# Kernel optimization log

Hardware: AMD Instinct MI355X
Metric: run time of the kernel (lower is better)

Reference implementation:

```python
import jax, jax.numpy as jnp
import numpy as np

COMMITMENT_COST = 0.25
NUM_EMBEDDINGS = 1024
EMBEDDING_DIM = 512  # win_size(8) * num_pellets(64)


def setup_inputs() -> dict:
    key = jax.random.key(0)
    k1, k2 = jax.random.split(key)
    inputs = jax.random.normal(k1, (64, 256, EMBEDDING_DIM), dtype=jnp.float32)
    # matches torch init: uniform_(-1/K, 1/K)
    lim = 1.0 / NUM_EMBEDDINGS
    emb_weight = jax.random.uniform(k2, (NUM_EMBEDDINGS, EMBEDDING_DIM),
                                    dtype=jnp.float32, minval=-lim, maxval=lim)
    return {"inputs": inputs, "emb_weight": emb_weight}


def reference(inputs, emb_weight):
    batch_size = inputs.shape[0]
    input_shape = inputs.shape
    flat = inputs.reshape(-1, EMBEDDING_DIM)  # [N, D]

    distances = (jnp.sum(flat * flat, axis=1, keepdims=True)
                 + jnp.sum(emb_weight * emb_weight, axis=1)
                 - 2.0 * flat @ emb_weight.T)
    encoding_indices = jnp.argmin(distances, axis=1)  # [N]

    # gather instead of one-hot matmul (same math)
    quantized = emb_weight[encoding_indices].reshape(input_shape)

    e_latent_loss = jnp.mean((jax.lax.stop_gradient(quantized) - inputs) ** 2)
    q_latent_loss = jnp.mean((quantized - jax.lax.stop_gradient(inputs)) ** 2)
    loss_vq = q_latent_loss + COMMITMENT_COST * e_latent_loss

    # straight-through estimator
    quantized = inputs + jax.lax.stop_gradient(quantized - inputs)

    encoding_indices = encoding_indices.reshape(batch_size, -1)
    return loss_vq, quantized, encoding_indices
```

## Files before the change

### kernel.cpp

```cpp
#include <hip/hip_runtime.h>
#include <cfloat>

#define NROWS  16384
#define DIM    512
#define KC     1024
#define QELEMS (NROWS * DIM)

#define NSPLIT 8
#define CHUNKS 130

typedef float  floatx4 __attribute__((ext_vector_type(4)));
typedef _Float16 half8 __attribute__((ext_vector_type(8)));
typedef _Float16 half4 __attribute__((ext_vector_type(4)));

__global__ __launch_bounds__(256) void prep_kernel(const float* __restrict__ A,
                                                   const float* __restrict__ E,
                                                   float* __restrict__ xsq,
                                                   float* __restrict__ esq,
                                                   _Float16* __restrict__ ah,
                                                   _Float16* __restrict__ al,
                                                   _Float16* __restrict__ eh,
                                                   _Float16* __restrict__ el,
                                                   unsigned long long* __restrict__ packed,
                                                   float* __restrict__ out) {
    if (blockIdx.x == 0 && threadIdx.x == 0) out[0] = 0.f;
    const int wave = threadIdx.x >> 6, lane = threadIdx.x & 63;
    const bool isA = blockIdx.x < (NROWS / 4);
    const int row = (isA ? blockIdx.x : blockIdx.x - NROWS / 4) * 4 + wave;
    const float* M = isA ? A : E;
    const float scale = isA ? 2048.0f : 65536.0f;

    const float4* Mr = (const float4*)(M + (size_t)row * DIM);
    float4 va = Mr[lane];
    float4 vb = Mr[lane + 64];
    float s = 0.f;
    s += va.x*va.x + va.y*va.y + va.z*va.z + va.w*va.w;
    s += vb.x*vb.x + vb.y*vb.y + vb.z*vb.z + vb.w*vb.w;
    #pragma unroll
    for (int off = 32; off; off >>= 1) s += __shfl_down(s, off, 64);
    if (lane == 0) {
        if (isA) { xsq[row] = s; packed[row] = ~0ULL; }
        else     { esq[row] = s; }
    }

    float xa[4] = {va.x, va.y, va.z, va.w}, xb[4] = {vb.x, vb.y, vb.z, vb.w};
    half4 ha, la, hb, lb;
    #pragma unroll
    for (int e = 0; e < 4; ++e) {
        float t = xa[e] * scale;
        _Float16 h = (_Float16)t;
        ha[e] = h; la[e] = (_Float16)(t - (float)h);
        t = xb[e] * scale;
        h = (_Float16)t;
        hb[e] = h; lb[e] = (_Float16)(t - (float)h);
    }
    _Float16* hr = (isA ? ah : eh) + (size_t)row * DIM;
    _Float16* lr = (isA ? al : el) + (size_t)row * DIM;
    ((half4*)hr)[lane]      = ha;
    ((half4*)lr)[lane]      = la;
    ((half4*)hr)[lane + 64] = hb;
    ((half4*)lr)[lane + 64] = lb;
}

__global__ __launch_bounds__(256, 3) void mfma_argmin_kernel(const _Float16* __restrict__ ah,
                                                             const _Float16* __restrict__ al,
                                                             const _Float16* __restrict__ eh,
                                                             const _Float16* __restrict__ el,
                                                             const float* __restrict__ esq,
                                                             const float* __restrict__ xsq,
                                                             unsigned long long* __restrict__ packed) {
    __shared__ half8 AhT[2][4 * CHUNKS], AlT[2][4 * CHUNKS];
    __shared__ float redv[128][2];
    __shared__ int   redi[128][2];

    const int tid = threadIdx.x;
    const int lane = tid & 63, wave = tid >> 6;
    const int wm = wave >> 1, wn = wave & 1;
    const int tx = lane & 15, qd = lane >> 4;
    const int bm = blockIdx.x & 127, bn = blockIdx.x >> 7;
    const int m0 = bm * 128, c0 = bn * 128;

    const int srow = tid >> 2, skq = tid & 3;
    const _Float16* gA  = ah + (size_t)(m0 + srow) * DIM + skq * 8;
    const _Float16* gAl = al + (size_t)(m0 + srow) * DIM + skq * 8;
    const int cw0 = skq * CHUNKS + srow, cw1 = cw0 + 64;

    const _Float16* gBh = eh + (size_t)(c0 + wn * 64 + tx) * DIM + qd * 8;
    const _Float16* gBl = el + (size_t)(c0 + wn * 64 + tx) * DIM + qd * 8;

    floatx4 acc[4][4];
    #pragma unroll
    for (int i = 0; i < 4; ++i)
        #pragma unroll
        for (int j = 0; j < 4; ++j) acc[i][j] = (floatx4){0.f, 0.f, 0.f, 0.f};

    half8 rA0 = *(const half8*)(gA);
    half8 rA1 = *(const half8*)(gA  + 64 * DIM);
    half8 rL0 = *(const half8*)(gAl);
    half8 rL1 = *(const half8*)(gAl + 64 * DIM);
    AhT[0][cw0] = rA0; AhT[0][cw1] = rA1;
    AlT[0][cw0] = rL0; AlT[0][cw1] = rL1;

    #pragma unroll 1
    for (int kt = 0; kt < DIM / 32; ++kt) {
        const int cur = kt & 1, nxt = cur ^ 1;
        const int kb = (kt + 1) * 32;
        const int ke = kt * 32;

        half8 fbh[4], fbl[4];
        #pragma unroll
        for (int j = 0; j < 4; ++j)
            fbh[j] = *(const half8*)(gBh + (size_t)j * 16 * DIM + ke);
        if (kt < DIM / 32 - 1) {
            rA0 = *(const half8*)(gA  + kb);
            rA1 = *(const half8*)(gA  + 64 * DIM + kb);
            rL0 = *(const half8*)(gAl + kb);
            rL1 = *(const half8*)(gAl + 64 * DIM + kb);
        }
        #pragma unroll
        for (int j = 0; j < 4; ++j)
            fbl[j] = *(const half8*)(gBl + (size_t)j * 16 * DIM + ke);
        __syncthreads();

        half8 fa[4];
        #pragma unroll
        for (int i = 0; i < 4; ++i)
            fa[i] = AhT[cur][qd * CHUNKS + wm * 64 + i * 16 + tx];
        #pragma unroll
        for (int i = 0; i < 4; ++i)
            #pragma unroll
            for (int j = 0; j < 4; ++j)
                acc[i][j] = __builtin_amdgcn_mfma_f32_16x16x32_f16(fa[i], fbh[j], acc[i][j], 0, 0, 0);
        #pragma unroll
        for (int i = 0; i < 4; ++i)
            #pragma unroll
            for (int j = 0; j < 4; ++j)
                acc[i][j] = __builtin_amdgcn_mfma_f32_16x16x32_f16(fa[i], fbl[j], acc[i][j], 0, 0, 0);
        #pragma unroll
        for (int i = 0; i < 4; ++i)
            fa[i] = AlT[cur][qd * CHUNKS + wm * 64 + i * 16 + tx];
        #pragma unroll
        for (int i = 0; i < 4; ++i)
            #pragma unroll
            for (int j = 0; j < 4; ++j)
                acc[i][j] = __builtin_amdgcn_mfma_f32_16x16x32_f16(fa[i], fbh[j], acc[i][j], 0, 0, 0);

        if (kt < DIM / 32 - 1) {
            AhT[nxt][cw0] = rA0; AhT[nxt][cw1] = rA1;
            AlT[nxt][cw0] = rL0; AlT[nxt][cw1] = rL1;
        }
    }

    float sqe_v[4];
    #pragma unroll
    for (int j = 0; j < 4; ++j) sqe_v[j] = esq[c0 + wn * 64 + j * 16 + tx];
    #pragma unroll
    for (int i = 0; i < 4; ++i) {
        #pragma unroll
        for (int r = 0; r < 4; ++r) {
            int rl = wm * 64 + i * 16 + qd * 4 + r;
            float sx = xsq[m0 + rl];
            float bvv = FLT_MAX; int bii = 0x7fffffff;
            #pragma unroll
            for (int j = 0; j < 4; ++j) {
                float S = sx + sqe_v[j];
                float s = S - acc[i][j][r] * (1.0f / 67108864.0f);
                int c = c0 + wn * 64 + j * 16 + tx;
                if (s < bvv || (s == bvv && c < bii)) { bvv = s; bii = c; }
            }
            #pragma unroll
            for (int md = 1; md < 16; md <<= 1) {
                float ov = __shfl_xor(bvv, md, 64);
                int   oc = __shfl_xor(bii, md, 64);
                if (ov < bvv || (ov == bvv && oc < bii)) { bvv = ov; bii = oc; }
            }
            if (tx == 0) { redv[rl][wn] = bvv; redi[rl][wn] = bii; }
        }
    }
    __syncthreads();
    if (tid < 128) {
        float v0 = redv[tid][0], v1 = redv[tid][1];
        int   i0 = redi[tid][0], i1 = redi[tid][1];
        float v = (v1 < v0) ? v1 : v0;
        int   ix = (v1 < v0) ? i1 : i0;
        unsigned long long pk = ((unsigned long long)__float_as_uint(v) << 32)
                              | (unsigned int)ix;
        atomicMin(&packed[m0 + tid], pk);
    }
}

__global__ __launch_bounds__(256) void finalize_kernel(const float* __restrict__ E,
                                                       const unsigned long long* __restrict__ packed,
                                                       float* __restrict__ out) {
    float* q = out + 1;
    float* idxF = out + 1 + QELEMS;
    const int tid = threadIdx.x;
    const int r0 = blockIdx.x * 16;

    __shared__ int sidx[16];
    if (tid < 64) {
        float sc = 0.f;
        if (tid < 16) {
            unsigned long long pk = packed[r0 + tid];
            int idx = (int)(unsigned int)(pk & 0xFFFFFFFFull);
            sc = __uint_as_float((unsigned int)(pk >> 32));
            sidx[tid] = idx;
            idxF[r0 + tid] = (float)idx;
        }
        #pragma unroll
        for (int off = 8; off; off >>= 1) sc += __shfl_down(sc, off, 16);
        if (tid == 0) atomicAdd(out, sc * (1.25f / (float)QELEMS));
    }
    __syncthreads();

    #pragma unroll 4
    for (int it = 0; it < 8; ++it) {
        int flat = it * 256 + tid;
        int row = flat >> 7;
        int d4  = (flat & 127) * 4;
        int idx = sidx[row];
        float4 e = *(const float4*)(E + (size_t)idx * DIM + d4);
        *(float4*)(q + (size_t)(r0 + row) * DIM + d4) = e;
    }
}

extern "C" void kernel_launch(void* const* d_in, const int* in_sizes, int n_in,
                              void* d_out, int out_size, void* d_ws, size_t ws_size,
                              hipStream_t stream) {
    const float* A = (const float*)d_in[0];
    const float* E = (const float*)d_in[1];
    float* out = (float*)d_out;

    unsigned long long* packed = (unsigned long long*)d_ws;
    float*    esq  = (float*)(packed + NROWS);
    float*    xsq  = esq + KC;
    _Float16* eh   = (_Float16*)(xsq + NROWS);
    _Float16* el   = eh + (size_t)KC * DIM;
    _Float16* ah   = el + (size_t)KC * DIM;
    _Float16* al   = ah + (size_t)NROWS * DIM;

    prep_kernel<<<NROWS / 4 + KC / 4, 256, 0, stream>>>(A, E, xsq, esq, ah, al, eh, el, packed, out);
    mfma_argmin_kernel<<<(NROWS / 128) * NSPLIT, 256, 0, stream>>>(
        ah, al, eh, el, esq, xsq, packed);
    finalize_kernel<<<NROWS / 16, 256, 0, stream>>>(E, packed, out);
}
```

Measured before the change: 187.6 us.

## Stage codebook tiles through LDS with two-deep register prefetch in the MFMA argmin

The codebook (E high/low halves) is now cooperatively loaded into shared memory alongside the input tiles, instead of each wave reading B fragments directly from global memory. The k-loop is unrolled by two with two register sets, so global loads run two tiles ahead of compute. s_setprio raises wave priority around the MFMA blocks. The extra LDS footprint and registers lower the occupancy hint from 3 to 2 blocks per CU, which may reduce latency hiding.

```diff
diff --git a/kernel.cpp b/kernel.cpp
--- a/kernel.cpp
+++ b/kernel.cpp
@@ -62,7 +62,58 @@
     ((half4*)lr)[lane + 64] = lb;
 }
 
-__global__ __launch_bounds__(256, 3) void mfma_argmin_kernel(const _Float16* __restrict__ ah,
+
+#define LOAD_SET(S, koff) \
+    S##A0 = *(const half8*)(gA  + (koff)); \
+    S##A1 = *(const half8*)(gA  + 64 * DIM + (koff)); \
+    S##L0 = *(const half8*)(gAl + (koff)); \
+    S##L1 = *(const half8*)(gAl + 64 * DIM + (koff)); \
+    S##E0 = *(const half8*)(gE  + (koff)); \
+    S##E1 = *(const half8*)(gE  + 64 * DIM + (koff)); \
+    S##F0 = *(const half8*)(gEl + (koff)); \
+    S##F1 = *(const half8*)(gEl + 64 * DIM + (koff));
+
+#define STORE_SET(S, b) \
+    AhT[b][cw0] = S##A0; AhT[b][cw1] = S##A1; \
+    AlT[b][cw0] = S##L0; AlT[b][cw1] = S##L1; \
+    EhT[b][cw0] = S##E0; EhT[b][cw1] = S##E1; \
+    ElT[b][cw0] = S##F0; ElT[b][cw1] = S##F1;
+
+#define COMPUTE(b) { \
+    half8 fa[4], fbh[4], fbl[4]; \
+    _Pragma("unroll") \
+    for (int i = 0; i < 4; ++i) \
+        fa[i] = AhT[b][qd * CHUNKS + wm * 64 + i * 16 + tx]; \
+    _Pragma("unroll") \
+    for (int j = 0; j < 4; ++j) { \
+        fbh[j] = EhT[b][qd * CHUNKS + wn * 64 + j * 16 + tx]; \
+        fbl[j] = ElT[b][qd * CHUNKS + wn * 64 + j * 16 + tx]; \
+    } \
+    __builtin_amdgcn_s_setprio(1); \
+    _Pragma("unroll") \
+    for (int i = 0; i < 4; ++i) \
+        _Pragma("unroll") \
+        for (int j = 0; j < 4; ++j) \
+            acc[i][j] = __builtin_amdgcn_mfma_f32_16x16x32_f16(fa[i], fbh[j], acc[i][j], 0, 0, 0); \
+    _Pragma("unroll") \
+    for (int i = 0; i < 4; ++i) \
+        _Pragma("unroll") \
+        for (int j = 0; j < 4; ++j) \
+            acc[i][j] = __builtin_amdgcn_mfma_f32_16x16x32_f16(fa[i], fbl[j], acc[i][j], 0, 0, 0); \
+    __builtin_amdgcn_s_setprio(0); \
+    _Pragma("unroll") \
+    for (int i = 0; i < 4; ++i) \
+        fa[i] = AlT[b][qd * CHUNKS + wm * 64 + i * 16 + tx]; \
+    __builtin_amdgcn_s_setprio(1); \
+    _Pragma("unroll") \
+    for (int i = 0; i < 4; ++i) \
+        _Pragma("unroll") \
+        for (int j = 0; j < 4; ++j) \
+            acc[i][j] = __builtin_amdgcn_mfma_f32_16x16x32_f16(fa[i], fbh[j], acc[i][j], 0, 0, 0); \
+    __builtin_amdgcn_s_setprio(0); \
+}
+
+__global__ __launch_bounds__(256, 2) void mfma_argmin_kernel(const _Float16* __restrict__ ah,
                                                              const _Float16* __restrict__ al,
                                                              const _Float16* __restrict__ eh,
                                                              const _Float16* __restrict__ el,
@@ -70,6 +121,7 @@
                                                              const float* __restrict__ xsq,
                                                              unsigned long long* __restrict__ packed) {
     __shared__ half8 AhT[2][4 * CHUNKS], AlT[2][4 * CHUNKS];
+    __shared__ half8 EhT[2][4 * CHUNKS], ElT[2][4 * CHUNKS];
     __shared__ float redv[128][2];
     __shared__ int   redi[128][2];
 
@@ -83,10 +135,9 @@
     const int srow = tid >> 2, skq = tid & 3;
     const _Float16* gA  = ah + (size_t)(m0 + srow) * DIM + skq * 8;
     const _Float16* gAl = al + (size_t)(m0 + srow) * DIM + skq * 8;
+    const _Float16* gE  = eh + (size_t)(c0 + srow) * DIM + skq * 8;
+    const _Float16* gEl = el + (size_t)(c0 + srow) * DIM + skq * 8;
     const int cw0 = skq * CHUNKS + srow, cw1 = cw0 + 64;
-
-    const _Float16* gBh = eh + (size_t)(c0 + wn * 64 + tx) * DIM + qd * 8;
-    const _Float16* gBl = el + (size_t)(c0 + wn * 64 + tx) * DIM + qd * 8;
 
     floatx4 acc[4][4];
     #pragma unroll
@@ -94,61 +145,24 @@
         #pragma unroll
         for (int j = 0; j < 4; ++j) acc[i][j] = (floatx4){0.f, 0.f, 0.f, 0.f};
 
-    half8 rA0 = *(const half8*)(gA);
-    half8 rA1 = *(const half8*)(gA  + 64 * DIM);
-    half8 rL0 = *(const half8*)(gAl);
-    half8 rL1 = *(const half8*)(gAl + 64 * DIM);
-    AhT[0][cw0] = rA0; AhT[0][cw1] = rA1;
-    AlT[0][cw0] = rL0; AlT[0][cw1] = rL1;
+    half8 pA0, pA1, pL0, pL1, pE0, pE1, pF0, pF1;
+    half8 qA0, qA1, qL0, qL1, qE0, qE1, qF0, qF1;
+
+    LOAD_SET(p, 0);
+    STORE_SET(p, 0);
+    LOAD_SET(q, 32);
 
     #pragma unroll 1
-    for (int kt = 0; kt < DIM / 32; ++kt) {
-        const int cur = kt & 1, nxt = cur ^ 1;
-        const int kb = (kt + 1) * 32;
-        const int ke = kt * 32;
-
-        half8 fbh[4], fbl[4];
-        #pragma unroll
-        for (int j = 0; j < 4; ++j)
-            fbh[j] = *(const half8*)(gBh + (size_t)j * 16 * DIM + ke);
-        if (kt < DIM / 32 - 1) {
-            rA0 = *(const half8*)(gA  + kb);
-            rA1 = *(const half8*)(gA  + 64 * DIM + kb);
-            rL0 = *(const half8*)(gAl + kb);
-            rL1 = *(const half8*)(gAl + 64 * DIM + kb);
-        }
-        #pragma unroll
-        for (int j = 0; j < 4; ++j)
-            fbl[j] = *(const half8*)(gBl + (size_t)j * 16 * DIM + ke);
+    for (int k2 = 0; k2 < 8; ++k2) {
+        const int kt = k2 * 2;
+        if (kt + 2 < 16) { LOAD_SET(p, (kt + 2) * 32); }
         __syncthreads();
-
-        half8 fa[4];
-        #pragma unroll
-        for (int i = 0; i < 4; ++i)
-            fa[i] = AhT[cur][qd * CHUNKS + wm * 64 + i * 16 + tx];
-        #pragma unroll
-        for (int i = 0; i < 4; ++i)
-            #pragma unroll
-            for (int j = 0; j < 4; ++j)
-                acc[i][j] = __builtin_amdgcn_mfma_f32_16x16x32_f16(fa[i], fbh[j], acc[i][j], 0, 0, 0);
-        #pragma unroll
-        for (int i = 0; i < 4; ++i)
-            #pragma unroll
-            for (int j = 0; j < 4; ++j)
-                acc[i][j] = __builtin_amdgcn_mfma_f32_16x16x32_f16(fa[i], fbl[j], acc[i][j], 0, 0, 0);
-        #pragma unroll
-        for (int i = 0; i < 4; ++i)
-            fa[i] = AlT[cur][qd * CHUNKS + wm * 64 + i * 16 + tx];
-        #pragma unroll
-        for (int i = 0; i < 4; ++i)
-            #pragma unroll
-            for (int j = 0; j < 4; ++j)
-                acc[i][j] = __builtin_amdgcn_mfma_f32_16x16x32_f16(fa[i], fbh[j], acc[i][j], 0, 0, 0);
-
-        if (kt < DIM / 32 - 1) {
-            AhT[nxt][cw0] = rA0; AhT[nxt][cw1] = rA1;
-            AlT[nxt][cw0] = rL0; AlT[nxt][cw1] = rL1;
-        }
+        COMPUTE(0);
+        STORE_SET(q, 1);
+        if (kt + 3 < 16) { LOAD_SET(q, (kt + 3) * 32); }
+        __syncthreads();
+        COMPUTE(1);
+        if (kt + 2 < 16) { STORE_SET(p, 0); }
     }
 
     float sqe_v[4];
```

New measurement: 179.2 us. 4.4% less time.
